# Performance work log

Measured on AMD Instinct MI355X. Metric: run time of the kernel, lower is better.

Reference implementation:

```python
import jax, jax.numpy as jnp
import numpy as np

B, D, H, NG = 8192, 2048, 2048, 7  # batch, input_size, hidden_size, num gate networks


def setup_inputs() -> dict:
    key = jax.random.key(0)
    ks = jax.random.split(key, 7)
    hx = jax.random.normal(ks[0], (B, D), dtype=jnp.float32)
    cx1 = jax.random.normal(ks[1], (B, H), dtype=jnp.float32)
    cx2 = jax.random.normal(ks[2], (B, H), dtype=jnp.float32)
    tj = jax.random.uniform(ks[3], (B, 1), dtype=jnp.float32)
    dt = jax.random.uniform(ks[4], (B, 1), dtype=jnp.float32)
    # fused weights for the 7 gate/decay networks, order: i1,i2,f1,f2,o,z,d
    W = jax.random.normal(ks[5], (D, NG * H), dtype=jnp.float32) * (1.0 / np.sqrt(D))
    b = jax.random.normal(ks[6], (NG * H,), dtype=jnp.float32) * 0.01
    return {"hx": hx, "cx1": cx1, "cx2": cx2, "tj": tj, "dt": dt, "W": W, "b": b}


def reference(hx, cx1, cx2, tj, dt, W, b):
    # One fused GEMM for all 7 gate networks, then split.
    g = hx @ W + b  # [B, 7H]
    i1, i2, f1, f2, o, z_raw, d_raw = [g[:, k * H:(k + 1) * H] for k in range(NG)]
    sig = jax.nn.sigmoid
    i1, i2, f1, f2, o = sig(i1), sig(i2), sig(f1), sig(f2), sig(o)
    z = jnp.tanh(z_raw)                 # Tanh(LC_z(hx)) as in forward
    decay = jax.nn.softplus(d_raw)      # Decay_network: positive decay coeff
    cy1 = f1 * cx1 + i1 * z             # fast cell state
    cy2 = f2 * cx2 + i2 * z             # asymptotic cell state
    t = tj + dt
    # continuous-time decay: c(t) = cy2 + (cy1 - cy2) * exp(-decay * (t - tj))
    c_t = cy2 + (cy1 - cy2) * jnp.exp(-decay * (t - tj))
    h_t = o * jnp.tanh(c_t)             # get_h(t)
    return jnp.stack([cy1, cy2, h_t])   # [3, B, H]
```

## Files before the change

kernel.cpp:

```cpp
#include <hip/hip_runtime.h>
#include <hip/hip_bf16.h>
#include <stdint.h>


#define B_SZ 8192
#define D_SZ 2048
#define H_SZ 2048
#define NG   7
#define NW   (NG * H_SZ)
#define BM   256
#define BN   32
#define BK   32
#define NKST (D_SZ / BK)
#define NBX  (B_SZ / BM)
#define NBY  (H_SZ / BN)

#define WB_BYTES   ((size_t)NBY * NKST * 14336)
#define HXB_OFF    WB_BYTES
#define HXB_BYTES  ((size_t)NBX * NKST * 16384)
#define WS_NEEDED  (WB_BYTES + HXB_BYTES)

typedef __attribute__((ext_vector_type(8))) short bf16x8;
typedef __attribute__((ext_vector_type(4))) float f32x4;

__device__ __forceinline__ uint32_t cvtpk(float lo, float hi) {
    uint32_t r;
    asm("v_cvt_pk_bf16_f32 %0, %1, %2" : "=v"(r) : "v"(lo), "v"(hi));
    return r;
}
__device__ __forceinline__ void glds16(const void* g, void* l) {
    __builtin_amdgcn_global_load_lds(
        (const __attribute__((address_space(1))) uint32_t*)g,
        (__attribute__((address_space(3))) uint32_t*)l, 16, 0, 0);
}
__device__ __forceinline__ float sigmoidf_(float x) {
    return 1.0f / (1.0f + __expf(-x));
}
__device__ __forceinline__ float tanhf_(float x) {
    float ax = fabsf(x);
    float e = __expf(2.0f * ax);
    float t = 1.0f - 2.0f / (e + 1.0f);
    return copysignf(t, x);
}
__device__ __forceinline__ float softplusf_(float x) {
    return (x > 30.0f) ? x : __logf(1.0f + __expf(x));
}

__global__ __launch_bounds__(896) void conv_w(const float* __restrict__ W,
                                              char* __restrict__ wb)
{
    const int by = blockIdx.x >> 6;
    const int ks = blockIdx.x & 63;
    const int u  = threadIdx.x;
    const int r  = u >> 2;
    const int pc = u & 3;
    const int koct = pc ^ ((r >> 1) & 3);
    const int g  = r >> 5;
    const int n  = r & 31;
    const int col = g * H_SZ + by * BN + n;
    const float* src = W + (size_t)(ks * BK + koct * 8) * NW + col;
    float w0 = src[0];
    float w1 = src[(size_t)NW];
    float w2 = src[(size_t)2 * NW];
    float w3 = src[(size_t)3 * NW];
    float w4 = src[(size_t)4 * NW];
    float w5 = src[(size_t)5 * NW];
    float w6 = src[(size_t)6 * NW];
    float w7 = src[(size_t)7 * NW];
    uint4 o;
    o.x = cvtpk(w0, w1); o.y = cvtpk(w2, w3);
    o.z = cvtpk(w4, w5); o.w = cvtpk(w6, w7);
    *(uint4*)(wb + (size_t)blockIdx.x * 14336 + u * 16) = o;
}

__global__ __launch_bounds__(1024) void conv_hx(const float* __restrict__ hx,
                                                char* __restrict__ hxb)
{
    const int bx = blockIdx.x >> 6;
    const int ks = blockIdx.x & 63;
    const int u  = threadIdx.x;
    const int r  = u >> 2;
    const int pc = u & 3;
    const int koct = pc ^ ((r >> 1) & 3);
    const float* src = hx + (size_t)(bx * BM + r) * D_SZ + ks * BK + koct * 8;
    f32x4 a = *(const f32x4*)(src);
    f32x4 b = *(const f32x4*)(src + 4);
    uint4 o;
    o.x = cvtpk(a[0], a[1]); o.y = cvtpk(a[2], a[3]);
    o.z = cvtpk(b[0], b[1]); o.w = cvtpk(b[2], b[3]);
    *(uint4*)(hxb + (size_t)blockIdx.x * 16384 + u * 16) = o;
}

#define NTH3 512
#define BUFB 30720
#define NBUF 4

#define PIPE_WAIT(N)                                        \
    asm volatile("s_waitcnt vmcnt(" #N ")" ::: "memory");   \
    __builtin_amdgcn_s_barrier();                           \
    asm volatile("" ::: "memory");

__global__ __launch_bounds__(NTH3, 2) void lstm_bf16(
    const char* __restrict__ wb, const char* __restrict__ hxb,
    const float* __restrict__ cx1, const float* __restrict__ cx2,
    const float* __restrict__ dt, const float* __restrict__ bias,
    float* __restrict__ out)
{
    __shared__ char smem[NBUF * BUFB];

    const int tid  = threadIdx.x;
    const int lane = tid & 63;
    const int wid  = tid >> 6;
    const int wm   = wid >> 1;
    const int wn   = wid & 1;
    const int l15  = lane & 15;
    const int lg   = lane >> 4;

    const int b0  = blockIdx.x;
    const int swz = (b0 & 7) * 256 + (b0 >> 3);
    const int by2 = swz >> 6;
    const int rem = swz & 63;
    const int bx  = rem >> 1;
    const int by  = by2 * 2 + (rem & 1);
    const int gm0 = bx * BM;
    const int n0  = by * BN;

    const size_t hx_tile0 = (size_t)(bx * NKST) << 14;
    const size_t w_tile0  = (size_t)(by * NKST) * 14336;

    const int xch  = (lg ^ ((l15 >> 1) & 3)) * 8;
    int aoff[4];
    #pragma unroll
    for (int mf = 0; mf < 4; ++mf)
        aoff[mf] = (wm * 64 + mf * 16 + l15) * 32 + xch;
    int boff[NG];
    #pragma unroll
    for (int g = 0; g < NG; ++g)
        boff[g] = (g * 32 + wn * 16 + l15) * 32 + xch;

    f32x4 acc[NG][4];
    #pragma unroll
    for (int g = 0; g < NG; ++g)
        #pragma unroll
        for (int mf = 0; mf < 4; ++mf)
            acc[g][mf] = (f32x4){0.f, 0.f, 0.f, 0.f};

    const int lane16 = lane << 4;

    auto stage = [&](int c, int k) {
        {
            const char* src = hxb + hx_tile0 + ((size_t)k << 14) + (wid << 11) + lane16;
            char* dst = smem + c * BUFB + (wid << 11);
            glds16(src, dst);
            glds16(src + 1024, dst + 1024);
        }
        {
            const char* src = wb + w_tile0 + (size_t)k * 14336 + wid * 1792 + lane16;
            char* dst = smem + c * BUFB + 16384 + wid * 1792;
            glds16(src, dst);
            if (lane < 48) glds16(src + 1024, dst + 1024);
        }
    };

    auto compute = [&](int c) {
        const ushort* sa = (const ushort*)(smem + c * BUFB);
        const ushort* sb = (const ushort*)(smem + c * BUFB + 16384);
        bf16x8 af[4];
        #pragma unroll
        for (int mf = 0; mf < 4; ++mf)
            af[mf] = *(const bf16x8*)(sa + aoff[mf]);
        __builtin_amdgcn_s_setprio(1);
        #pragma unroll
        for (int g = 0; g < NG; ++g) {
            bf16x8 bfr = *(const bf16x8*)(sb + boff[g]);
            #pragma unroll
            for (int mf = 0; mf < 4; ++mf)
                acc[g][mf] = __builtin_amdgcn_mfma_f32_16x16x32_bf16(
                    af[mf], bfr, acc[g][mf], 0, 0, 0);
        }
        __builtin_amdgcn_s_setprio(0);
    };

    stage(0, 0);
    stage(1, 1);
    stage(2, 2);

    for (int t = 0; t < NKST - 3; ++t) {
        PIPE_WAIT(8)
        stage((t + 3) & 3, t + 3);
        compute(t & 3);
    }
    PIPE_WAIT(8)
    compute((NKST - 3) & 3);
    PIPE_WAIT(4)
    compute((NKST - 2) & 3);
    PIPE_WAIT(0)
    compute((NKST - 1) & 3);

    const size_t BH = (size_t)B_SZ * H_SZ;
    const int j = n0 + wn * 16 + l15;
    float bj[NG];
    #pragma unroll
    for (int g = 0; g < NG; ++g) bj[g] = bias[g * H_SZ + j];

    #pragma unroll
    for (int mf = 0; mf < 4; ++mf) {
        #pragma unroll
        for (int r = 0; r < 4; ++r) {
            int row = gm0 + wm * 64 + mf * 16 + lg * 4 + r;
            float dtv = dt[row];
            float i1 = sigmoidf_(acc[0][mf][r] + bj[0]);
            float i2 = sigmoidf_(acc[1][mf][r] + bj[1]);
            float f1 = sigmoidf_(acc[2][mf][r] + bj[2]);
            float f2 = sigmoidf_(acc[3][mf][r] + bj[3]);
            float o  = sigmoidf_(acc[4][mf][r] + bj[4]);
            float z  = tanhf_(acc[5][mf][r] + bj[5]);
            float dec = softplusf_(acc[6][mf][r] + bj[6]);
            size_t idx = (size_t)row * H_SZ + j;
            float c1 = cx1[idx], c2 = cx2[idx];
            float cy1 = f1 * c1 + i1 * z;
            float cy2 = f2 * c2 + i2 * z;
            float ct  = cy2 + (cy1 - cy2) * __expf(-dec * dtv);
            float ht  = o * tanhf_(ct);
            out[idx]          = cy1;
            out[BH + idx]     = cy2;
            out[2 * BH + idx] = ht;
        }
    }
}

#define NTH  512
#define LDP  40
__global__ __launch_bounds__(NTH, 2) void lstm_f32(
    const float* __restrict__ hx, const float* __restrict__ cx1,
    const float* __restrict__ cx2, const float* __restrict__ dt,
    const float* __restrict__ W, const float* __restrict__ bias,
    float* __restrict__ out)
{
    __shared__ ushort sA[BM * LDP];
    __shared__ ushort sB[NG * BN * LDP];

    const int tid = threadIdx.x;
    const int nwg = gridDim.x;
    const int cpx = nwg >> 3;
    const int b0  = blockIdx.x;
    const int swz = (b0 & 7) * cpx + (b0 >> 3);
    const int bx  = swz & 31;
    const int by  = swz >> 5;
    const int gm0 = bx * BM;
    const int n0  = by * BN;

    const int lane = tid & 63;
    const int wid  = tid >> 6;
    const int wm   = wid >> 1;
    const int wn   = wid & 1;
    const int l15  = lane & 15;
    const int lg   = lane >> 4;

    const int ar0 = tid >> 2,          aq0 = tid & 3;
    const int ar1 = (tid + 512) >> 2,  aq1 = tid & 3;
    const bool hasB = (tid < 448);
    const int bg  = tid >> 6;
    const int bkq = (tid >> 3) & 7;
    const int bnq = tid & 7;

    f32x4 pa[4];
    f32x4 pb[4];

    auto issue_loads = [&](int K0) {
        {
            const float* p = hx + (size_t)(gm0 + ar0) * D_SZ + K0 + aq0 * 8;
            pa[0] = *(const f32x4*)(p);
            pa[1] = *(const f32x4*)(p + 4);
        }
        {
            const float* p = hx + (size_t)(gm0 + ar1) * D_SZ + K0 + aq1 * 8;
            pa[2] = *(const f32x4*)(p);
            pa[3] = *(const f32x4*)(p + 4);
        }
        if (hasB) {
            const float* p = W + (size_t)(K0 + bkq * 4) * NW + bg * H_SZ + n0 + bnq * 4;
            pb[0] = *(const f32x4*)(p);
            pb[1] = *(const f32x4*)(p + NW);
            pb[2] = *(const f32x4*)(p + 2 * NW);
            pb[3] = *(const f32x4*)(p + 3 * NW);
        }
    };

    auto store_lds = [&]() {
        {
            uint4 u;
            u.x = cvtpk(pa[0][0], pa[0][1]); u.y = cvtpk(pa[0][2], pa[0][3]);
            u.z = cvtpk(pa[1][0], pa[1][1]); u.w = cvtpk(pa[1][2], pa[1][3]);
            *(uint4*)(&sA[ar0 * LDP + aq0 * 8]) = u;
        }
        {
            uint4 u;
            u.x = cvtpk(pa[2][0], pa[2][1]); u.y = cvtpk(pa[2][2], pa[2][3]);
            u.z = cvtpk(pa[3][0], pa[3][1]); u.w = cvtpk(pa[3][2], pa[3][3]);
            *(uint4*)(&sA[ar1 * LDP + aq1 * 8]) = u;
        }
        if (hasB) {
            #pragma unroll
            for (int jj = 0; jj < 4; ++jj) {
                uint2 v;
                v.x = cvtpk(pb[0][jj], pb[1][jj]);
                v.y = cvtpk(pb[2][jj], pb[3][jj]);
                *(uint2*)(&sB[(bg * BN + bnq * 4 + jj) * LDP + bkq * 4]) = v;
            }
        }
    };

    f32x4 acc[NG][4];
    #pragma unroll
    for (int g = 0; g < NG; ++g)
        #pragma unroll
        for (int mf = 0; mf < 4; ++mf)
            acc[g][mf] = (f32x4){0.f, 0.f, 0.f, 0.f};

    int aoff[4];
    #pragma unroll
    for (int mf = 0; mf < 4; ++mf)
        aoff[mf] = (wm * 64 + mf * 16 + l15) * LDP + lg * 8;
    int boff[NG];
    #pragma unroll
    for (int g = 0; g < NG; ++g)
        boff[g] = (g * BN + wn * 16 + l15) * LDP + lg * 8;

    issue_loads(0);
    for (int kk = 0; kk < NKST; ++kk) {
        store_lds();
        __syncthreads();
        if (kk + 1 < NKST) issue_loads((kk + 1) * BK);

        bf16x8 af[4];
        #pragma unroll
        for (int mf = 0; mf < 4; ++mf)
            af[mf] = *(const bf16x8*)(&sA[aoff[mf]]);
        #pragma unroll
        for (int g = 0; g < NG; ++g) {
            bf16x8 bfr = *(const bf16x8*)(&sB[boff[g]]);
            #pragma unroll
            for (int mf = 0; mf < 4; ++mf)
                acc[g][mf] = __builtin_amdgcn_mfma_f32_16x16x32_bf16(
                    af[mf], bfr, acc[g][mf], 0, 0, 0);
        }
        __syncthreads();
    }

    const size_t BH = (size_t)B_SZ * H_SZ;
    const int j = n0 + wn * 16 + l15;
    float bj[NG];
    #pragma unroll
    for (int g = 0; g < NG; ++g) bj[g] = bias[g * H_SZ + j];

    #pragma unroll
    for (int mf = 0; mf < 4; ++mf) {
        #pragma unroll
        for (int r = 0; r < 4; ++r) {
            int row = gm0 + wm * 64 + mf * 16 + lg * 4 + r;
            float dtv = dt[row];
            float i1 = sigmoidf_(acc[0][mf][r] + bj[0]);
            float i2 = sigmoidf_(acc[1][mf][r] + bj[1]);
            float f1 = sigmoidf_(acc[2][mf][r] + bj[2]);
            float f2 = sigmoidf_(acc[3][mf][r] + bj[3]);
            float o  = sigmoidf_(acc[4][mf][r] + bj[4]);
            float z  = tanhf_(acc[5][mf][r] + bj[5]);
            float dec = softplusf_(acc[6][mf][r] + bj[6]);
            size_t idx = (size_t)row * H_SZ + j;
            float c1 = cx1[idx], c2 = cx2[idx];
            float cy1 = f1 * c1 + i1 * z;
            float cy2 = f2 * c2 + i2 * z;
            float ct  = cy2 + (cy1 - cy2) * __expf(-dec * dtv);
            float ht  = o * tanhf_(ct);
            out[idx]          = cy1;
            out[BH + idx]     = cy2;
            out[2 * BH + idx] = ht;
        }
    }
}

extern "C" void kernel_launch(void* const* d_in, const int* in_sizes, int n_in,
                              void* d_out, int out_size, void* d_ws, size_t ws_size,
                              hipStream_t stream) {
    const float* hx  = (const float*)d_in[0];
    const float* cx1 = (const float*)d_in[1];
    const float* cx2 = (const float*)d_in[2];
    const float* dt  = (const float*)d_in[4];
    const float* W   = (const float*)d_in[5];
    const float* b   = (const float*)d_in[6];
    float* out = (float*)d_out;

    if (ws_size >= WS_NEEDED) {
        char* wb  = (char*)d_ws;
        char* hxb = (char*)d_ws + HXB_OFF;
        conv_w<<<dim3(NBY * NKST), dim3(896), 0, stream>>>(W, wb);
        conv_hx<<<dim3(NBX * NKST), dim3(1024), 0, stream>>>(hx, hxb);
        lstm_bf16<<<dim3(NBX * NBY), dim3(NTH3), 0, stream>>>(
            wb, hxb, cx1, cx2, dt, b, out);
    } else {
        lstm_f32<<<dim3(NBX * NBY), dim3(NTH), 0, stream>>>(
            hx, cx1, cx2, dt, W, b, out);
    }
}
```

Baseline: 553.6 us.

## Double-buffer LDS fragments in registers to overlap reads with MFMA

Restructures the main GEMM loop so the LDS fragment loads for the next k-step go into a second register set while MFMAs run on the current one. The loop is unrolled by two with alternating even/odd fragment sets, and four stages are issued up front instead of three. The goal is to hide LDS read latency behind matrix-core work. It raises register pressure (two fragment sets of 11 bf16x8 each) under a 2-waves launch bound, and the wait macro now also drains lgkmcnt at each barrier.

```diff
diff --git a/kernel.cpp b/kernel.cpp
--- a/kernel.cpp
+++ b/kernel.cpp
@@ -95,10 +95,12 @@
 #define BUFB 30720
 #define NBUF 4
 
-#define PIPE_WAIT(N)                                        \
-    asm volatile("s_waitcnt vmcnt(" #N ")" ::: "memory");   \
-    __builtin_amdgcn_s_barrier();                           \
-    asm volatile("" ::: "memory");
+#define PIPE_WAIT(N)                                                    \
+    asm volatile("s_waitcnt vmcnt(" #N ") lgkmcnt(0)" ::: "memory");    \
+    __builtin_amdgcn_s_barrier();                                       \
+    __builtin_amdgcn_sched_barrier(0);
+
+struct Frags { bf16x8 a[4]; bf16x8 b[NG]; };
 
 __global__ __launch_bounds__(NTH3, 2) void lstm_bf16(
     const char* __restrict__ wb, const char* __restrict__ hxb,
@@ -162,40 +164,61 @@
         }
     };
 
-    auto compute = [&](int c) {
+    auto prefetch = [&](int c, Frags& f) {
         const ushort* sa = (const ushort*)(smem + c * BUFB);
         const ushort* sb = (const ushort*)(smem + c * BUFB + 16384);
-        bf16x8 af[4];
         #pragma unroll
         for (int mf = 0; mf < 4; ++mf)
-            af[mf] = *(const bf16x8*)(sa + aoff[mf]);
+            f.a[mf] = *(const bf16x8*)(sa + aoff[mf]);
+        #pragma unroll
+        for (int g = 0; g < NG; ++g)
+            f.b[g] = *(const bf16x8*)(sb + boff[g]);
+    };
+
+    auto compute = [&](const Frags& f) {
         __builtin_amdgcn_s_setprio(1);
         #pragma unroll
-        for (int g = 0; g < NG; ++g) {
-            bf16x8 bfr = *(const bf16x8*)(sb + boff[g]);
+        for (int g = 0; g < NG; ++g)
             #pragma unroll
             for (int mf = 0; mf < 4; ++mf)
                 acc[g][mf] = __builtin_amdgcn_mfma_f32_16x16x32_bf16(
-                    af[mf], bfr, acc[g][mf], 0, 0, 0);
-        }
+                    f.a[mf], f.b[g], acc[g][mf], 0, 0, 0);
         __builtin_amdgcn_s_setprio(0);
     };
 
     stage(0, 0);
     stage(1, 1);
     stage(2, 2);
-
-    for (int t = 0; t < NKST - 3; ++t) {
+    stage(3, 3);
+    asm volatile("s_waitcnt vmcnt(12)" ::: "memory");
+    __builtin_amdgcn_s_barrier();
+    __builtin_amdgcn_sched_barrier(0);
+
+    Frags fE, fO;
+    prefetch(0, fE);
+
+    for (int t = 0; t < NKST - 4; t += 2) {
         PIPE_WAIT(8)
-        stage((t + 3) & 3, t + 3);
-        compute(t & 3);
+        stage(t & 3, t + 4);
+        prefetch((t + 1) & 3, fO);
+        compute(fE);
+        PIPE_WAIT(8)
+        stage((t + 1) & 3, t + 5);
+        prefetch((t + 2) & 3, fE);
+        compute(fO);
     }
     PIPE_WAIT(8)
-    compute((NKST - 3) & 3);
+    prefetch(61 & 3, fO);
+    compute(fE);
     PIPE_WAIT(4)
-    compute((NKST - 2) & 3);
+    prefetch(62 & 3, fE);
+    compute(fO);
     PIPE_WAIT(0)
-    compute((NKST - 1) & 3);
+    prefetch(63 & 3, fO);
+    compute(fE);
+    asm volatile("s_waitcnt lgkmcnt(0)" ::: "memory");
+    __builtin_amdgcn_sched_barrier(0);
+    compute(fO);
 
     const size_t BH = (size_t)B_SZ * H_SZ;
     const int j = n0 + wn * 16 + l15;
```

Measured after the change: 553.2 us. No clear change (-0.1%).

## Prefetch next k-step LDS fragments into double-buffered registers during MFMA clusters

Applied to the files above, without the earlier changes.

Restructures the main loop so that each k-step's A and B fragments for the next step are read from LDS into ping-pong register arrays while the current step's MFMA clusters run. Scheduling barriers pin each per-row-fragment MFMA cluster in place so LDS reads interleave with matrix math. The global-load wait is tightened from vmcnt(8) to vmcnt(4), so the stage for step t+1 must land before step t computes. The aim is to hide LDS read latency behind MFMAs. The cost is one fewer load stage in flight and about 56 extra registers per thread, which risks spills or lower occupancy under the 2-block launch bound.

```diff
diff --git a/kernel.cpp b/kernel.cpp
--- a/kernel.cpp
+++ b/kernel.cpp
@@ -95,10 +95,11 @@
 #define BUFB 30720
 #define NBUF 4
 
+#define SB0 __builtin_amdgcn_sched_barrier(0)
 #define PIPE_WAIT(N)                                        \
     asm volatile("s_waitcnt vmcnt(" #N ")" ::: "memory");   \
     __builtin_amdgcn_s_barrier();                           \
-    asm volatile("" ::: "memory");
+    __builtin_amdgcn_sched_barrier(0);
 
 __global__ __launch_bounds__(NTH3, 2) void lstm_bf16(
     const char* __restrict__ wb, const char* __restrict__ hxb,
@@ -162,40 +163,67 @@
         }
     };
 
-    auto compute = [&](int c) {
-        const ushort* sa = (const ushort*)(smem + c * BUFB);
-        const ushort* sb = (const ushort*)(smem + c * BUFB + 16384);
-        bf16x8 af[4];
-        #pragma unroll
-        for (int mf = 0; mf < 4; ++mf)
-            af[mf] = *(const bf16x8*)(sa + aoff[mf]);
-        __builtin_amdgcn_s_setprio(1);
-        #pragma unroll
-        for (int g = 0; g < NG; ++g) {
-            bf16x8 bfr = *(const bf16x8*)(sb + boff[g]);
+    bf16x8 bfE[NG], bfO[NG];
+    bf16x8 af0, af1, af2, af3;
+
+    #define MFMA_CLUSTER(BFC, AF, P)                                        \
+        SB0;                                                                \
+        __builtin_amdgcn_s_setprio(1);                                      \
+        _Pragma("unroll")                                                   \
+        for (int g = 0; g < NG; ++g)                                        \
+            acc[g][P] = __builtin_amdgcn_mfma_f32_16x16x32_bf16(            \
+                AF, BFC[g], acc[g][P], 0, 0, 0);                            \
+        __builtin_amdgcn_s_setprio(0);                                      \
+        SB0;
+
+    auto phases = [&](int t, bf16x8 (&bfC)[NG], bf16x8 (&bfN)[NG], bool doPre) {
+        const ushort* sa  = (const ushort*)(smem + (t & 3) * BUFB);
+        const ushort* saN = (const ushort*)(smem + ((t + 1) & 3) * BUFB);
+        const ushort* sbN = (const ushort*)(smem + ((t + 1) & 3) * BUFB + 16384);
+        af1 = *(const bf16x8*)(sa + aoff[1]);
+        MFMA_CLUSTER(bfC, af0, 0)
+        af2 = *(const bf16x8*)(sa + aoff[2]);
+        MFMA_CLUSTER(bfC, af1, 1)
+        af3 = *(const bf16x8*)(sa + aoff[3]);
+        MFMA_CLUSTER(bfC, af2, 2)
+        if (doPre) {
             #pragma unroll
-            for (int mf = 0; mf < 4; ++mf)
-                acc[g][mf] = __builtin_amdgcn_mfma_f32_16x16x32_bf16(
-                    af[mf], bfr, acc[g][mf], 0, 0, 0);
-        }
-        __builtin_amdgcn_s_setprio(0);
+            for (int g = 0; g < NG; ++g)
+                bfN[g] = *(const bf16x8*)(sbN + boff[g]);
+            af0 = *(const bf16x8*)(saN + aoff[0]);
+        }
+        MFMA_CLUSTER(bfC, af3, 3)
     };
 
     stage(0, 0);
     stage(1, 1);
     stage(2, 2);
-
-    for (int t = 0; t < NKST - 3; ++t) {
-        PIPE_WAIT(8)
+    PIPE_WAIT(4)
+    {
+        const ushort* sa0 = (const ushort*)(smem);
+        const ushort* sb0 = (const ushort*)(smem + 16384);
+        #pragma unroll
+        for (int g = 0; g < NG; ++g)
+            bfE[g] = *(const bf16x8*)(sb0 + boff[g]);
+        af0 = *(const bf16x8*)(sa0 + aoff[0]);
+    }
+
+    for (int t = 0; t < 60; t += 2) {
+        PIPE_WAIT(4)
         stage((t + 3) & 3, t + 3);
-        compute(t & 3);
-    }
-    PIPE_WAIT(8)
-    compute((NKST - 3) & 3);
+        phases(t, bfE, bfO, true);
+        PIPE_WAIT(4)
+        stage((t + 4) & 3, t + 4);
+        phases(t + 1, bfO, bfE, true);
+    }
     PIPE_WAIT(4)
-    compute((NKST - 2) & 3);
+    stage(63 & 3, 63);
+    phases(60, bfE, bfO, true);
+    PIPE_WAIT(4)
+    phases(61, bfO, bfE, true);
     PIPE_WAIT(0)
-    compute((NKST - 1) & 3);
+    phases(62, bfE, bfO, true);
+    phases(63, bfO, bfE, false);
 
     const size_t BH = (size_t)B_SZ * H_SZ;
     const int j = n0 + wn * 16 + l15;
```

New measurement: 557.1 us. About the same (+0.6%).

## Shrink bf16 GEMM block tile to 128 rows with 3-stage LDS pipeline

Applied to the files above, without the earlier changes.

Halves the M tile of the fused bf16 GEMM to 128 rows, uses 256-thread blocks, and replaces the 4-buffer LDS ring with a 3-buffer ring and an unrolled-by-three main loop. The hx pre-conversion kernel is retiled to match, and the block swizzle is simplified. This doubles the block count and cuts LDS per block, aiming at higher occupancy and better latency hiding. In exchange each weight tile is reused over fewer rows, so weight traffic per FLOP goes up.

```diff
diff --git a/kernel.cpp b/kernel.cpp
--- a/kernel.cpp
+++ b/kernel.cpp
@@ -8,16 +8,16 @@
 #define H_SZ 2048
 #define NG   7
 #define NW   (NG * H_SZ)
-#define BM   256
+#define BMW  128
 #define BN   32
 #define BK   32
 #define NKST (D_SZ / BK)
-#define NBX  (B_SZ / BM)
+#define NBXW (B_SZ / BMW)
 #define NBY  (H_SZ / BN)
 
 #define WB_BYTES   ((size_t)NBY * NKST * 14336)
 #define HXB_OFF    WB_BYTES
-#define HXB_BYTES  ((size_t)NBX * NKST * 16384)
+#define HXB_BYTES  ((size_t)NBXW * NKST * 8192)
 #define WS_NEEDED  (WB_BYTES + HXB_BYTES)
 
 typedef __attribute__((ext_vector_type(8))) short bf16x8;
@@ -73,8 +73,8 @@
     *(uint4*)(wb + (size_t)blockIdx.x * 14336 + u * 16) = o;
 }
 
-__global__ __launch_bounds__(1024) void conv_hx(const float* __restrict__ hx,
-                                                char* __restrict__ hxb)
+__global__ __launch_bounds__(512) void conv_hx(const float* __restrict__ hx,
+                                               char* __restrict__ hxb)
 {
     const int bx = blockIdx.x >> 6;
     const int ks = blockIdx.x & 63;
@@ -82,18 +82,17 @@
     const int r  = u >> 2;
     const int pc = u & 3;
     const int koct = pc ^ ((r >> 1) & 3);
-    const float* src = hx + (size_t)(bx * BM + r) * D_SZ + ks * BK + koct * 8;
+    const float* src = hx + (size_t)(bx * BMW + r) * D_SZ + ks * BK + koct * 8;
     f32x4 a = *(const f32x4*)(src);
     f32x4 b = *(const f32x4*)(src + 4);
     uint4 o;
     o.x = cvtpk(a[0], a[1]); o.y = cvtpk(a[2], a[3]);
     o.z = cvtpk(b[0], b[1]); o.w = cvtpk(b[2], b[3]);
-    *(uint4*)(hxb + (size_t)blockIdx.x * 16384 + u * 16) = o;
-}
-
-#define NTH3 512
-#define BUFB 30720
-#define NBUF 4
+    *(uint4*)(hxb + (size_t)blockIdx.x * 8192 + u * 16) = o;
+}
+
+#define NTH3 256
+#define BUFB 22528
 
 #define PIPE_WAIT(N)                                        \
     asm volatile("s_waitcnt vmcnt(" #N ")" ::: "memory");   \
@@ -106,7 +105,7 @@
     const float* __restrict__ dt, const float* __restrict__ bias,
     float* __restrict__ out)
 {
-    __shared__ char smem[NBUF * BUFB];
+    __shared__ char smem[3 * BUFB];
 
     const int tid  = threadIdx.x;
     const int lane = tid & 63;
@@ -117,18 +116,16 @@
     const int lg   = lane >> 4;
 
     const int b0  = blockIdx.x;
-    const int swz = (b0 & 7) * 256 + (b0 >> 3);
-    const int by2 = swz >> 6;
-    const int rem = swz & 63;
-    const int bx  = rem >> 1;
-    const int by  = by2 * 2 + (rem & 1);
-    const int gm0 = bx * BM;
+    const int swz = (b0 & 7) * 512 + (b0 >> 3);
+    const int bx  = swz & 63;
+    const int by  = swz >> 6;
+    const int gm0 = bx * BMW;
     const int n0  = by * BN;
 
-    const size_t hx_tile0 = (size_t)(bx * NKST) << 14;
-    const size_t w_tile0  = (size_t)(by * NKST) * 14336;
-
-    const int xch  = (lg ^ ((l15 >> 1) & 3)) * 8;
+    const int hx_t0 = bx * NKST;
+    const int w_t0  = by * NKST;
+
+    const int xch = (lg ^ ((l15 >> 1) & 3)) * 8;
     int aoff[4];
     #pragma unroll
     for (int mf = 0; mf < 4; ++mf)
@@ -136,7 +133,7 @@
     int boff[NG];
     #pragma unroll
     for (int g = 0; g < NG; ++g)
-        boff[g] = (g * 32 + wn * 16 + l15) * 32 + xch;
+        boff[g] = 4096 + (g * 32 + wn * 16 + l15) * 32 + xch;
 
     f32x4 acc[NG][4];
     #pragma unroll
@@ -149,26 +146,27 @@
 
     auto stage = [&](int c, int k) {
         {
-            const char* src = hxb + hx_tile0 + ((size_t)k << 14) + (wid << 11) + lane16;
-            char* dst = smem + c * BUFB + (wid << 11);
-            glds16(src, dst);
-            glds16(src + 1024, dst + 1024);
-        }
-        {
-            const char* src = wb + w_tile0 + (size_t)k * 14336 + wid * 1792 + lane16;
-            char* dst = smem + c * BUFB + 16384 + wid * 1792;
-            glds16(src, dst);
-            if (lane < 48) glds16(src + 1024, dst + 1024);
+            const char* s = hxb + ((size_t)(hx_t0 + k) << 13) + (wid << 11) + lane16;
+            char* d = smem + c * BUFB + (wid << 11);
+            glds16(s, d);
+            glds16(s + 1024, d + 1024);
+        }
+        {
+            const char* s = wb + (size_t)(w_t0 + k) * 14336 + wid * 3584 + lane16;
+            char* d = smem + c * BUFB + 8192 + wid * 3584;
+            glds16(s, d);
+            glds16(s + 1024, d + 1024);
+            glds16(s + 2048, d + 2048);
+            if (lane < 32) glds16(s + 3072, d + 3072);
         }
     };
 
     auto compute = [&](int c) {
-        const ushort* sa = (const ushort*)(smem + c * BUFB);
-        const ushort* sb = (const ushort*)(smem + c * BUFB + 16384);
+        const ushort* sb = (const ushort*)(smem + c * BUFB);
         bf16x8 af[4];
         #pragma unroll
         for (int mf = 0; mf < 4; ++mf)
-            af[mf] = *(const bf16x8*)(sa + aoff[mf]);
+            af[mf] = *(const bf16x8*)(sb + aoff[mf]);
         __builtin_amdgcn_s_setprio(1);
         #pragma unroll
         for (int g = 0; g < NG; ++g) {
@@ -183,19 +181,29 @@
 
     stage(0, 0);
     stage(1, 1);
-    stage(2, 2);
-
-    for (int t = 0; t < NKST - 3; ++t) {
-        PIPE_WAIT(8)
-        stage((t + 3) & 3, t + 3);
-        compute(t & 3);
+
+    #pragma unroll 1
+    for (int it = 0; it < 20; ++it) {
+        PIPE_WAIT(6)
+        stage(2, (it * 3) + 2);
+        compute(0);
+        PIPE_WAIT(6)
+        stage(0, (it * 3) + 3);
+        compute(1);
+        PIPE_WAIT(6)
+        stage(1, (it * 3) + 4);
+        compute(2);
     }
-    PIPE_WAIT(8)
-    compute((NKST - 3) & 3);
-    PIPE_WAIT(4)
-    compute((NKST - 2) & 3);
+    PIPE_WAIT(6)
+    stage(2, 62);
+    compute(0);
+    PIPE_WAIT(6)
+    stage(0, 63);
+    compute(1);
+    PIPE_WAIT(6)
+    compute(2);
     PIPE_WAIT(0)
-    compute((NKST - 1) & 3);
+    compute(0);
 
     const size_t BH = (size_t)B_SZ * H_SZ;
     const int j = n0 + wn * 16 + l15;
@@ -229,6 +237,7 @@
     }
 }
 
+#define BM   256
 #define NTH  512
 #define LDP  40
 __global__ __launch_bounds__(NTH, 2) void lstm_f32(
@@ -395,11 +404,11 @@
         char* wb  = (char*)d_ws;
         char* hxb = (char*)d_ws + HXB_OFF;
         conv_w<<<dim3(NBY * NKST), dim3(896), 0, stream>>>(W, wb);
-        conv_hx<<<dim3(NBX * NKST), dim3(1024), 0, stream>>>(hx, hxb);
-        lstm_bf16<<<dim3(NBX * NBY), dim3(NTH3), 0, stream>>>(
+        conv_hx<<<dim3(NBXW * NKST), dim3(512), 0, stream>>>(hx, hxb);
+        lstm_bf16<<<dim3(NBXW * NBY), dim3(NTH3), 0, stream>>>(
             wb, hxb, cx1, cx2, dt, b, out);
     } else {
-        lstm_f32<<<dim3(NBX * NBY), dim3(NTH), 0, stream>>>(
+        lstm_f32<<<dim3((B_SZ / BM) * NBY), dim3(NTH), 0, stream>>>(
             hx, cx1, cx2, dt, W, b, out);
     }
 }
```

Result: no change. 549.7 us (-0.7%).
